# Optimization experiments

Hardware: AMD Instinct MI355X
Metric: run time of the kernel (lower is better)

Reference implementation:

```python
import jax, jax.numpy as jnp
import numpy as np

NUM_USERS = 100_000
NUM_ITEMS = 50_000
N = NUM_USERS + NUM_ITEMS
DIM = 64
HOP = 3
NNZ = 3_200_000
BATCH = 4096


def setup_inputs() -> dict:
    key = jax.random.key(0)
    k = jax.random.split(key, 8)
    edge_row = jax.random.randint(k[0], (NNZ,), 0, N, dtype=jnp.int32)
    edge_col = jax.random.randint(k[1], (NNZ,), 0, N, dtype=jnp.int32)
    # normalized-Laplacian-like small positive values (~1/deg)
    edge_val = jax.random.uniform(k[2], (NNZ,), dtype=jnp.float32) * 0.05
    # xavier_normal-ish init for embedding tables
    std = (2.0 / (NUM_USERS + DIM)) ** 0.5
    user_emb = jax.random.normal(k[3], (NUM_USERS, DIM), dtype=jnp.float32) * 0.1
    item_emb = jax.random.normal(k[4], (NUM_ITEMS, DIM), dtype=jnp.float32) * 0.1
    users = jax.random.randint(k[5], (BATCH,), 0, NUM_USERS, dtype=jnp.int32)
    items = jax.random.randint(k[6], (BATCH,), 0, NUM_ITEMS, dtype=jnp.int32)
    negatives = jax.random.randint(k[7], (BATCH,), 0, NUM_ITEMS, dtype=jnp.int32)
    return {"edge_row": edge_row, "edge_col": edge_col, "edge_val": edge_val,
            "user_emb": user_emb, "item_emb": item_emb,
            "users": users, "items": items, "negatives": negatives}


def _spmm(edge_row, edge_col, edge_val, x):
    # y[r] = sum_e val[e] * x[col[e]]  (COO SpMM)
    msgs = edge_val[:, None] * x[edge_col]          # [nnz, d]
    return jax.ops.segment_sum(msgs, edge_row, num_segments=N)


def reference(edge_row, edge_col, edge_val, user_emb, item_emb, users, items, negatives):
    all_emb = jnp.concatenate((user_emb, item_emb), axis=0)   # [N, d]
    acc = all_emb
    x = all_emb
    for _ in range(HOP):
        x = _spmm(edge_row, edge_col, edge_val, x)
        acc = acc + x
    light_out = acc / jnp.float32(HOP + 1)                     # mean over hop+1 layers
    all_users_emb = light_out[:NUM_USERS]
    all_items_emb = light_out[NUM_USERS:]
    users_emb = all_users_emb[users]                           # [B, d]
    items_emb = all_items_emb[items]                           # [B, d]
    neg_item_emb = all_items_emb[negatives]                    # [B, d]
    pos_scores = jnp.sum(users_emb * items_emb, axis=1)
    neg_scores = jnp.sum(users_emb * neg_item_emb, axis=1)
    bpr_loss = jnp.mean(jax.nn.softplus(neg_scores - pos_scores))
    return bpr_loss
```

## Files before the change

kernel.cpp:

```cpp
#include <hip/hip_runtime.h>
#include <hip/hip_bf16.h>
#include <math.h>

#define NUM_USERS 100000
#define NUM_ITEMS 50000
#define N_NODES   (NUM_USERS + NUM_ITEMS)
#define DIM       64
#define NNZ_      3200000
#define BATCH_    4096

#define COLMASK 0x3FFFF

#define SB_ROWS 1024
#define NSB     147
#define SBCAP   24576
#define PBCAP   (SBCAP + SB_ROWS * 7)

#define P1_EPB  4096
#define P1_BLOCKS ((NNZ_ + P1_EPB - 1) / P1_EPB)

#define VAL_SCALE  327680.0f
#define VAL_INV    (0.05f / 16384.0f)

typedef __attribute__((ext_vector_type(2))) float f32x2;


__device__ __forceinline__ unsigned pk4_fp8(float a, float b, float c, float d) {
    int w = __builtin_amdgcn_cvt_pk_fp8_f32(a, b, 0, false);
    w     = __builtin_amdgcn_cvt_pk_fp8_f32(c, d, w, true);
    return (unsigned)w;
}
__device__ __forceinline__ float dec8(unsigned byte) {
    return __builtin_amdgcn_cvt_f32_fp8((int)byte, 0);
}


__global__ void init_cursors(int* __restrict__ cursor1) {
    int i = blockIdx.x * 256 + threadIdx.x;
    if (i < NSB) cursor1[i] = i * SBCAP;
}


__global__ void part1(const int* __restrict__ erow, const int* __restrict__ ecol,
                      const float* __restrict__ eval_, int* __restrict__ cursor1,
                      int2* __restrict__ cpairs1) {
    __shared__ int h[NSB];
    __shared__ int bs[NSB];
    int t = threadIdx.x;
    int start = blockIdx.x * P1_EPB;
    int end = start + P1_EPB; if (end > NNZ_) end = NNZ_;

    if (t < NSB) h[t] = 0;
    __syncthreads();
    for (int i = start + t; i < end; i += 256)
        atomicAdd(&h[erow[i] >> 10], 1);
    __syncthreads();
    if (t < NSB) { int c = h[t]; bs[t] = c ? atomicAdd(&cursor1[t], c) : 0; }
    __syncthreads();
    if (t < NSB) h[t] = 0;
    __syncthreads();

    for (int i0 = start + t; i0 < end; i0 += 1024) {
        int r[4], c[4]; float v[4];
        #pragma unroll
        for (int k = 0; k < 4; ++k) {
            int idx = i0 + k * 256;
            if (idx < end) { r[k] = erow[idx]; c[k] = ecol[idx]; v[k] = eval_[idx]; }
            else r[k] = -1;
        }
        #pragma unroll
        for (int k = 0; k < 4; ++k) {
            if (r[k] >= 0) {
                int sb = r[k] >> 10;
                int pos = bs[sb] + atomicAdd(&h[sb], 1);
                cpairs1[pos] = make_int2(((r[k] & (SB_ROWS - 1)) << 18) | c[k],
                                         __float_as_int(v[k]));
            }
        }
    }
}


#define SORT_THREADS 1024

__global__ void sort_sb(const int* __restrict__ cursor1, const int2* __restrict__ cpairs1,
                        int* __restrict__ rowptrP, int* __restrict__ rowendP,
                        unsigned* __restrict__ pairs) {
    __shared__ int hist[SB_ROWS];
    __shared__ int offs[SB_ROWS];
    __shared__ int curs[SB_ROWS];
    int t = threadIdx.x;
    int sb = blockIdx.x;
    int beg = sb * SBCAP;
    int end = cursor1[sb];
    int pbase = sb * PBCAP;

    hist[t] = 0;
    __syncthreads();
    for (int i = beg + t; i < end; i += SORT_THREADS)
        atomicAdd(&hist[(cpairs1[i].x >> 18) & (SB_ROWS - 1)], 1);
    __syncthreads();
    int pc = (hist[t] + 7) & ~7;
    curs[t] = pc;
    __syncthreads();
    for (int off = 1; off < SB_ROWS; off <<= 1) {
        int v = (t >= off) ? curs[t - off] : 0;
        __syncthreads();
        curs[t] += v;
        __syncthreads();
    }
    int pex = curs[t] - pc;
    offs[t] = pex;
    {
        int row = sb * SB_ROWS + t;
        if (row < N_NODES) {
            rowptrP[row] = pbase + pex;
            rowendP[row] = pbase + pex + pc;
        }
    }
    __syncthreads();
    curs[t] = 0;
    __syncthreads();
    for (int i = beg + t; i < end; i += SORT_THREADS) {
        int2 p = cpairs1[i];
        int rl = (p.x >> 18) & (SB_ROWS - 1);
        int pos = pbase + offs[rl] + atomicAdd(&curs[rl], 1);
        unsigned vfix = (unsigned)fminf(__int_as_float(p.y) * VAL_SCALE + 0.5f, 16383.0f);
        pairs[pos] = ((unsigned)(p.x & COLMASK) << 14) | vfix;
    }
    __syncthreads();
    {
        int c = hist[t];
        int pcc = (c + 7) & ~7;
        int b2 = pbase + offs[t];
        for (int j = c; j < pcc; ++j) pairs[b2 + j] = 0u;
    }
}


__global__ void cvt_fp8(const float* __restrict__ ue, const float* __restrict__ ie,
                        unsigned* __restrict__ ef8) {
    int i = blockIdx.x * blockDim.x + threadIdx.x;
    const int NQ = N_NODES * DIM / 4;
    if (i >= NQ) return;
    const int UQ = NUM_USERS * DIM / 4;
    float4 v = (i < UQ) ? ((const float4*)ue)[i] : ((const float4*)ie)[i - UQ];
    ef8[i] = pk4_fp8(v.x, v.y, v.z, v.w);
}


__global__ void spmm_csr(const int* __restrict__ rowptrP, const int* __restrict__ rowendP,
                         const unsigned* __restrict__ pairs,
                         const unsigned char* __restrict__ x, unsigned char* __restrict__ out) {
    int w    = (blockIdx.x * blockDim.x + threadIdx.x) >> 6;
    int lane = threadIdx.x & 63;
    if (w >= N_NODES) return;
    int q   = lane >> 4;
    int sub = lane & 15;
    int beg = rowptrP[w], end = rowendP[w];

    float a0 = 0.f, a1 = 0.f, a2 = 0.f, a3 = 0.f;
    float b0 = 0.f, b1 = 0.f, b2 = 0.f, b3 = 0.f;

    int base = beg + q;
    if ((end - beg) & 8) {
        unsigned pA = pairs[base];
        unsigned pB = pairs[base + 4];
        unsigned vA = *(const unsigned*)(x + (size_t)(pA >> 14) * DIM + 4 * sub);
        unsigned vB = *(const unsigned*)(x + (size_t)(pB >> 14) * DIM + 4 * sub);
        float sA = (float)(pA & 0x3FFFu) * VAL_INV;
        float sB = (float)(pB & 0x3FFFu) * VAL_INV;
        f32x2 loA = __builtin_amdgcn_cvt_pk_f32_fp8((int)vA, false);
        f32x2 hiA = __builtin_amdgcn_cvt_pk_f32_fp8((int)vA, true);
        f32x2 loB = __builtin_amdgcn_cvt_pk_f32_fp8((int)vB, false);
        f32x2 hiB = __builtin_amdgcn_cvt_pk_f32_fp8((int)vB, true);
        a0 = fmaf(sA, loA.x, a0); a1 = fmaf(sA, loA.y, a1);
        a2 = fmaf(sA, hiA.x, a2); a3 = fmaf(sA, hiA.y, a3);
        b0 = fmaf(sB, loB.x, b0); b1 = fmaf(sB, loB.y, b1);
        b2 = fmaf(sB, hiB.x, b2); b3 = fmaf(sB, hiB.y, b3);
        base += 8;
    }
    for (; base < end; base += 16) {
        unsigned p0 = pairs[base];
        unsigned p1 = pairs[base + 4];
        unsigned p2 = pairs[base + 8];
        unsigned p3 = pairs[base + 12];
        unsigned v0 = *(const unsigned*)(x + (size_t)(p0 >> 14) * DIM + 4 * sub);
        unsigned v1 = *(const unsigned*)(x + (size_t)(p1 >> 14) * DIM + 4 * sub);
        unsigned v2 = *(const unsigned*)(x + (size_t)(p2 >> 14) * DIM + 4 * sub);
        unsigned v3 = *(const unsigned*)(x + (size_t)(p3 >> 14) * DIM + 4 * sub);
        float s0 = (float)(p0 & 0x3FFFu) * VAL_INV;
        float s1 = (float)(p1 & 0x3FFFu) * VAL_INV;
        float s2 = (float)(p2 & 0x3FFFu) * VAL_INV;
        float s3 = (float)(p3 & 0x3FFFu) * VAL_INV;
        f32x2 lo0 = __builtin_amdgcn_cvt_pk_f32_fp8((int)v0, false);
        f32x2 hi0 = __builtin_amdgcn_cvt_pk_f32_fp8((int)v0, true);
        f32x2 lo1 = __builtin_amdgcn_cvt_pk_f32_fp8((int)v1, false);
        f32x2 hi1 = __builtin_amdgcn_cvt_pk_f32_fp8((int)v1, true);
        f32x2 lo2 = __builtin_amdgcn_cvt_pk_f32_fp8((int)v2, false);
        f32x2 hi2 = __builtin_amdgcn_cvt_pk_f32_fp8((int)v2, true);
        f32x2 lo3 = __builtin_amdgcn_cvt_pk_f32_fp8((int)v3, false);
        f32x2 hi3 = __builtin_amdgcn_cvt_pk_f32_fp8((int)v3, true);
        a0 = fmaf(s0, lo0.x, a0); a1 = fmaf(s0, lo0.y, a1);
        a2 = fmaf(s0, hi0.x, a2); a3 = fmaf(s0, hi0.y, a3);
        b0 = fmaf(s1, lo1.x, b0); b1 = fmaf(s1, lo1.y, b1);
        b2 = fmaf(s1, hi1.x, b2); b3 = fmaf(s1, hi1.y, b3);
        a0 = fmaf(s2, lo2.x, a0); a1 = fmaf(s2, lo2.y, a1);
        a2 = fmaf(s2, hi2.x, a2); a3 = fmaf(s2, hi2.y, a3);
        b0 = fmaf(s3, lo3.x, b0); b1 = fmaf(s3, lo3.y, b1);
        b2 = fmaf(s3, hi3.x, b2); b3 = fmaf(s3, hi3.y, b3);
    }
    a0 += b0; a1 += b1; a2 += b2; a3 += b3;

    a0 += __shfl_xor(a0, 16); a0 += __shfl_xor(a0, 32);
    a1 += __shfl_xor(a1, 16); a1 += __shfl_xor(a1, 32);
    a2 += __shfl_xor(a2, 16); a2 += __shfl_xor(a2, 32);
    a3 += __shfl_xor(a3, 16); a3 += __shfl_xor(a3, 32);

    if (lane < 16) {
        *(unsigned*)(out + (size_t)w * DIM + 4 * sub) = pk4_fp8(a0, a1, a2, a3);
    }
}


__device__ __forceinline__ float emb0(const float* __restrict__ ue,
                                      const float* __restrict__ ie,
                                      int node, int lane) {
    return (node < NUM_USERS) ? ue[(size_t)node * DIM + lane]
                              : ie[(size_t)(node - NUM_USERS) * DIM + lane];
}

__device__ __forceinline__ float hop3(const int* __restrict__ rowptrP,
                                      const int* __restrict__ rowendP,
                                      const unsigned* __restrict__ pairs,
                                      const unsigned char* __restrict__ h2, int node, int lane) {
    int beg = rowptrP[node], end = rowendP[node];
    float a0 = 0.f, a1 = 0.f, a2 = 0.f, a3 = 0.f;
    for (int base = beg; base < end; base += 8) {
        unsigned p[8];
        #pragma unroll
        for (int k = 0; k < 8; ++k) p[k] = pairs[base + k];
        float xv[8];
        #pragma unroll
        for (int k = 0; k < 8; ++k)
            xv[k] = dec8(h2[(size_t)(p[k] >> 14) * DIM + lane]);
        a0 = fmaf((float)(p[0] & 0x3FFFu) * VAL_INV, xv[0], a0);
        a1 = fmaf((float)(p[1] & 0x3FFFu) * VAL_INV, xv[1], a1);
        a2 = fmaf((float)(p[2] & 0x3FFFu) * VAL_INV, xv[2], a2);
        a3 = fmaf((float)(p[3] & 0x3FFFu) * VAL_INV, xv[3], a3);
        a0 = fmaf((float)(p[4] & 0x3FFFu) * VAL_INV, xv[4], a0);
        a1 = fmaf((float)(p[5] & 0x3FFFu) * VAL_INV, xv[5], a1);
        a2 = fmaf((float)(p[6] & 0x3FFFu) * VAL_INV, xv[6], a2);
        a3 = fmaf((float)(p[7] & 0x3FFFu) * VAL_INV, xv[7], a3);
    }
    return (a0 + a1) + (a2 + a3);
}

__global__ void score_fused(const float* __restrict__ ue, const float* __restrict__ ie,
                            const unsigned char* __restrict__ h1,
                            const unsigned char* __restrict__ h2,
                            const int* __restrict__ rowptrP, const int* __restrict__ rowendP,
                            const unsigned* __restrict__ pairs,
                            const int* __restrict__ users, const int* __restrict__ items,
                            const int* __restrict__ negs,
                            float* __restrict__ out) {
    __shared__ float vecs[3][DIM];
    int b    = blockIdx.x;
    int role = threadIdx.x >> 6;
    int lane = threadIdx.x & 63;

    int node = (role == 0) ? users[b]
             : (role == 1) ? NUM_USERS + items[b]
                           : NUM_USERS + negs[b];

    size_t o = (size_t)node * DIM + lane;
    float v = emb0(ue, ie, node, lane) + dec8(h1[o]) + dec8(h2[o]) +
              hop3(rowptrP, rowendP, pairs, h2, node, lane);
    vecs[role][lane] = v;
    __syncthreads();

    if (role == 0) {
        float u   = v;
        float pos = u * vecs[1][lane];
        float neg = u * vecs[2][lane];
        #pragma unroll
        for (int s = 32; s >= 1; s >>= 1) {
            pos += __shfl_xor(pos, s);
            neg += __shfl_xor(neg, s);
        }
        if (lane == 0) {
            float x = (neg - pos) * (1.0f / 16.0f);
            float sp = fmaxf(x, 0.0f) + log1pf(expf(-fabsf(x)));
            atomicAdd(out, sp * (1.0f / BATCH_));
        }
    }
}


extern "C" void kernel_launch(void* const* d_in, const int* in_sizes, int n_in,
                              void* d_out, int out_size, void* d_ws, size_t ws_size,
                              hipStream_t stream) {
    const int*   edge_row  = (const int*)d_in[0];
    const int*   edge_col  = (const int*)d_in[1];
    const float* edge_val  = (const float*)d_in[2];
    const float* user_emb  = (const float*)d_in[3];
    const float* item_emb  = (const float*)d_in[4];
    const int*   users     = (const int*)d_in[5];
    const int*   items     = (const int*)d_in[6];
    const int*   negatives = (const int*)d_in[7];
    float* out = (float*)d_out;

    int* w = (int*)d_ws;
    int*  cursor1 = w;
    int*  rowptrP = cursor1 + NSB + 1;
    int*  rowendP = rowptrP + N_NODES;
    int2*     cpairs1 = (int2*)(rowendP + N_NODES);
    unsigned* pairs   = (unsigned*)(cpairs1 + (size_t)NSB * SBCAP);
    unsigned* ef8     = pairs + (size_t)NSB * PBCAP;
    unsigned* h1w     = ef8 + (size_t)N_NODES * DIM / 4;
    unsigned* h2w     = h1w + (size_t)N_NODES * DIM / 4;

    hipMemsetAsync(d_out, 0, sizeof(float), stream);

    const int blk = 256;
    const int cvtBlocks = (N_NODES * DIM / 4 + blk - 1) / blk;
    const int rowWaveBlocks = (N_NODES * 64 + blk - 1) / blk;

    init_cursors<<<1, blk, 0, stream>>>(cursor1);
    part1<<<P1_BLOCKS, blk, 0, stream>>>(edge_row, edge_col, edge_val, cursor1, cpairs1);
    sort_sb<<<NSB, SORT_THREADS, 0, stream>>>(cursor1, cpairs1, rowptrP, rowendP, pairs);
    cvt_fp8<<<cvtBlocks, blk, 0, stream>>>(user_emb, item_emb, ef8);

    spmm_csr<<<rowWaveBlocks, blk, 0, stream>>>(rowptrP, rowendP, pairs,
                                                (const unsigned char*)ef8, (unsigned char*)h1w);
    spmm_csr<<<rowWaveBlocks, blk, 0, stream>>>(rowptrP, rowendP, pairs,
                                                (const unsigned char*)h1w, (unsigned char*)h2w);

    score_fused<<<BATCH_, 192, 0, stream>>>(user_emb, item_emb,
                                            (const unsigned char*)h1w,
                                            (const unsigned char*)h2w,
                                            rowptrP, rowendP, pairs,
                                            users, items, negatives, out);
}
```

Baseline: 276.1 us.

## Stage partitioned edges in shared memory for coalesced bucket writes

The first-pass partition kernel now keeps each thread's row indices in registers instead of reading them twice. It computes a block-local prefix over bucket counts and scatters edges into a shared-memory staging buffer grouped by bucket. It then writes the staged data out contiguously per bucket, finding each element's bucket with a binary search. This targets the scattered 8-byte global writes of the original, at the cost of 32KB of LDS per block, an extra scan, and a binary search per output element.

```diff
diff --git a/kernel.cpp b/kernel.cpp
--- a/kernel.cpp
+++ b/kernel.cpp
@@ -44,39 +44,71 @@
 __global__ void part1(const int* __restrict__ erow, const int* __restrict__ ecol,
                       const float* __restrict__ eval_, int* __restrict__ cursor1,
                       int2* __restrict__ cpairs1) {
-    __shared__ int h[NSB];
-    __shared__ int bs[NSB];
+    __shared__ int  h[NSB];
+    __shared__ int  bs[NSB];
+    __shared__ int  loff[NSB + 1];
+    __shared__ int  scn[256];
+    __shared__ int2 stage[P1_EPB];
     int t = threadIdx.x;
     int start = blockIdx.x * P1_EPB;
     int end = start + P1_EPB; if (end > NNZ_) end = NNZ_;
+    int total = end - start;
 
     if (t < NSB) h[t] = 0;
     __syncthreads();
-    for (int i = start + t; i < end; i += 256)
-        atomicAdd(&h[erow[i] >> 10], 1);
-    __syncthreads();
-    if (t < NSB) { int c = h[t]; bs[t] = c ? atomicAdd(&cursor1[t], c) : 0; }
+
+    int rows[16];
+    #pragma unroll
+    for (int i = 0; i < 16; ++i) {
+        int idx = start + i * 256 + t;
+        rows[i] = (idx < end) ? erow[idx] : -1;
+        if (rows[i] >= 0) atomicAdd(&h[rows[i] >> 10], 1);
+    }
+    __syncthreads();
+
+    int c0 = (t < NSB) ? h[t] : 0;
+    scn[t] = c0;
+    __syncthreads();
+    for (int off = 1; off < 256; off <<= 1) {
+        int v = (t >= off) ? scn[t - off] : 0;
+        __syncthreads();
+        scn[t] += v;
+        __syncthreads();
+    }
+    if (t <= NSB) loff[t] = (t == 0) ? 0 : scn[t - 1];
+    if (t < NSB && c0) bs[t] = atomicAdd(&cursor1[t], c0);
     __syncthreads();
     if (t < NSB) h[t] = 0;
     __syncthreads();
 
-    for (int i0 = start + t; i0 < end; i0 += 1024) {
-        int r[4], c[4]; float v[4];
+    #pragma unroll
+    for (int i0 = 0; i0 < 16; i0 += 4) {
+        int c[4]; float v[4];
         #pragma unroll
         for (int k = 0; k < 4; ++k) {
-            int idx = i0 + k * 256;
-            if (idx < end) { r[k] = erow[idx]; c[k] = ecol[idx]; v[k] = eval_[idx]; }
-            else r[k] = -1;
+            int idx = start + (i0 + k) * 256 + t;
+            if (idx < end) { c[k] = ecol[idx]; v[k] = eval_[idx]; }
         }
         #pragma unroll
         for (int k = 0; k < 4; ++k) {
-            if (r[k] >= 0) {
-                int sb = r[k] >> 10;
-                int pos = bs[sb] + atomicAdd(&h[sb], 1);
-                cpairs1[pos] = make_int2(((r[k] & (SB_ROWS - 1)) << 18) | c[k],
-                                         __float_as_int(v[k]));
+            int r = rows[i0 + k];
+            if (r >= 0) {
+                int b = r >> 10;
+                int pos = loff[b] + atomicAdd(&h[b], 1);
+                stage[pos] = make_int2(((r & (SB_ROWS - 1)) << 18) | c[k],
+                                       __float_as_int(v[k]));
             }
         }
+    }
+    __syncthreads();
+
+    for (int k = t; k < total; k += 256) {
+        int lo = 0, hi = NSB;
+        while (hi - lo > 1) {
+            int mid = (lo + hi) >> 1;
+            if (k >= loff[mid]) lo = mid; else hi = mid;
+        }
+        cpairs1[bs[lo] + (k - loff[lo])] = stage[k];
     }
 }
 
```

Measured after the change: 272.2 us. Within noise of the previous version (-1.4%).
